# Kernel optimization log

Hardware: AMD Instinct MI355X
Metric: run time of the kernel (lower is better)

Reference implementation:

```python
import jax, jax.numpy as jnp
import numpy as np

N, D_IN, D_OUT, NHEAD = 4096, 512, 128, 4


def setup_inputs() -> dict:
    key = jax.random.key(0)
    k1, k2, k3, k4, k5 = jax.random.split(key, 5)
    adj = jax.random.randint(k1, (N, N), 0, 2).astype(jnp.float32)  # dense binary adjacency
    x = jax.random.normal(k2, (N, D_IN), dtype=jnp.float32)
    W = jax.random.normal(k3, (D_IN, D_OUT), dtype=jnp.float32) * (1.0 / np.sqrt(D_IN))
    attn_l_w = jax.random.normal(k4, (NHEAD, D_OUT), dtype=jnp.float32) * (1.0 / np.sqrt(D_OUT))
    attn_r_w = jax.random.normal(k5, (NHEAD, D_OUT), dtype=jnp.float32) * (1.0 / np.sqrt(D_OUT))
    b = jnp.zeros((D_OUT,), dtype=jnp.float32)
    return {"adj": adj, "x": x, "W": W, "attn_l_w": attn_l_w, "attn_r_w": attn_r_w, "b": b}


def reference(adj, x, W, attn_l_w, attn_r_w, b):
    # h = x @ W : [N, D_OUT]
    h = x @ W
    el = h @ attn_l_w.T  # [N, H]  (nn.Linear(output_dim, nhead, bias=False))
    er = h @ attn_r_w.T  # [N, H]
    # Dense equivalent of nonzero-gather + index_put_ scatter into [N, N, H]:
    # attn[i, j, :] = exp(leaky_relu(el[i] + er[j])) where adj[i, j] != 0, else 0.
    e = el[:, None, :] + er[None, :, :]                      # [N, N, H]
    a = jnp.where(adj[:, :, None] != 0,
                  jnp.exp(jax.nn.leaky_relu(e, negative_slope=0.2)),
                  jnp.zeros((), dtype=e.dtype))              # [N, N, H]
    a = jnp.transpose(a, (0, 2, 1))                          # [N, H, N]
    # F.normalize(p=1, dim=-1): divide by max(L1 row sum, 1e-12); a >= 0 so L1 = sum.
    a = a / jnp.maximum(jnp.sum(a, axis=-1, keepdims=True), 1e-12)
    out = jnp.einsum('nhm,md->nhd', a, h) + b                # [N, H, D_OUT]
    return out.reshape(out.shape[0], -1)                     # flatten heads -> [N, H*D_OUT]
```

## Files before the change

kernel.cpp:

```cpp
#include <hip/hip_runtime.h>

#define NN 4096
#define DIN 512
#define DOUT 128
#define NH 4
#define LOG2E 1.44269504088896340736f

typedef __bf16 bf16x8 __attribute__((ext_vector_type(8)));
typedef float f32x4 __attribute__((ext_vector_type(4)));
typedef float f32x16 __attribute__((ext_vector_type(16)));
typedef unsigned short u16;
typedef unsigned int u32;
typedef u16 u16x8 __attribute__((ext_vector_type(8)));
typedef u16 u16x4 __attribute__((ext_vector_type(4)));

static __device__ __forceinline__ u16 f2bf(float f) {
  __bf16 h = (__bf16)f;
  return __builtin_bit_cast(u16, h);
}

static __device__ __forceinline__ void gl_lds16(const void* g, void* l) {
  __builtin_amdgcn_global_load_lds(
      (const __attribute__((address_space(1))) unsigned int*)g,
      (__attribute__((address_space(3))) unsigned int*)l, 16, 0, 0);
}

__global__ __launch_bounds__(256) void pack_prep(const float* __restrict__ adj,
                                                 u32* __restrict__ adjW,
                                                 const float* __restrict__ W,
                                                 u16* __restrict__ wthi,
                                                 u16* __restrict__ wtlo) {
  const int b = blockIdx.x;
  const int t = threadIdx.x;
  if (b < 2048) {
    const int idx = b * 256 + t;
    const float4* src = (const float4*)(adj + (size_t)idx * 32);
    u32 m = 0;
    #pragma unroll
    for (int c = 0; c < 8; ++c) {
      const float4 v = src[c];
      m |= (v.x != 0.f ? 1u : 0u) << (c * 4);
      m |= (v.y != 0.f ? 2u : 0u) << (c * 4);
      m |= (v.z != 0.f ? 4u : 0u) << (c * 4);
      m |= (v.w != 0.f ? 8u : 0u) << (c * 4);
    }
    adjW[idx] = m;
  } else {
    const int n = b - 2048;
    for (int k = t; k < 512; k += 256) {
      const float w = W[(size_t)k * 128 + n];
      const __bf16 hi = (__bf16)w;
      wthi[(size_t)n * 512 + k] = __builtin_bit_cast(u16, hi);
      wtlo[(size_t)n * 512 + k] = f2bf(w - (float)hi);
    }
  }
}

__global__ __launch_bounds__(512, 1) void hcompute(
    const float* __restrict__ x, const u16* __restrict__ wthi,
    const u16* __restrict__ wtlo, const float* __restrict__ alw,
    const float* __restrict__ arw, u16* __restrict__ hT,
    float* __restrict__ el, float* __restrict__ erT) {
  __shared__ __align__(16) char pool[147456];
  const int t = threadIdx.x;
  const int i0 = blockIdx.x * 16;
  const int lane = t & 63, w = t >> 6;
  const int l15 = lane & 15, lhi = lane >> 4;

  const int xr = t >> 5, xk = (t & 31) * 4;
  const unsigned x_off =
      ((unsigned)(xr * 256 + xk * 2)) ^ ((unsigned)((xr & 7) << 4));

  f32x4 acc = (f32x4){0.f, 0.f, 0.f, 0.f};

  auto stageW = [&](int kc, int buf) {
    #pragma unroll
    for (int q = 0; q < 4; ++q) {
      const int off = q * 8192 + t * 16;
      const int n = off >> 8;
      const int kb = off & 255;
      const int ksrc = (kb ^ ((n & 7) << 4)) >> 1;
      const size_t so = (size_t)n * 512 + kc * 128 + ksrc;
      gl_lds16(wthi + so, pool + 16384 + buf * 32768 + off);
      gl_lds16(wtlo + so, pool + 81920 + buf * 32768 + off);
    }
  };
  auto writeX = [&](const float4& xv, int buf) {
    u16x4 hi, lo;
    const float* xp = (const float*)&xv;
    #pragma unroll
    for (int j = 0; j < 4; ++j) {
      const __bf16 hb = (__bf16)xp[j];
      hi[j] = __builtin_bit_cast(u16, hb);
      lo[j] = f2bf(xp[j] - (float)hb);
    }
    *(u16x4*)(pool + buf * 4096 + x_off) = hi;
    *(u16x4*)(pool + 8192 + buf * 4096 + x_off) = lo;
  };

  stageW(0, 0);
  {
    float4 xv = *(const float4*)(x + (size_t)(i0 + xr) * DIN + xk);
    writeX(xv, 0);
  }
  float4 xnext;
  for (int kc = 0; kc < 4; ++kc) {
    const int cur = kc & 1;
    __syncthreads();
    const bool more = (kc < 3);
    if (more) {
      stageW(kc + 1, cur ^ 1);
      xnext = *(const float4*)(x + (size_t)(i0 + xr) * DIN + (kc + 1) * 128 + xk);
    }
    #pragma unroll
    for (int ks = 0; ks < 4; ++ks) {
      const unsigned kbyte = (unsigned)(ks * 64 + lhi * 16);
      const unsigned xoff =
          (unsigned)(l15 * 256) + (kbyte ^ (unsigned)((l15 & 7) << 4));
      const bf16x8 ah = *(const bf16x8*)(pool + cur * 4096 + xoff);
      const bf16x8 al = *(const bf16x8*)(pool + 8192 + cur * 4096 + xoff);
      const int n = w * 16 + l15;
      const unsigned wb =
          (unsigned)(n * 256) + (kbyte ^ (unsigned)((n & 7) << 4));
      const bf16x8 bh = *(const bf16x8*)(pool + 16384 + cur * 32768 + wb);
      const bf16x8 bl = *(const bf16x8*)(pool + 81920 + cur * 32768 + wb);
      acc = __builtin_amdgcn_mfma_f32_16x16x32_bf16(ah, bh, acc, 0, 0, 0);
      acc = __builtin_amdgcn_mfma_f32_16x16x32_bf16(al, bh, acc, 0, 0, 0);
      acc = __builtin_amdgcn_mfma_f32_16x16x32_bf16(ah, bl, acc, 0, 0, 0);
    }
    if (more) writeX(xnext, cur ^ 1);
  }
  __syncthreads();
  float* h_lds = (float*)(pool + 16384);
  #pragma unroll
  for (int reg = 0; reg < 4; ++reg)
    h_lds[(lhi * 4 + reg) * 132 + w * 16 + l15] = acc[reg];
  __syncthreads();
  {
    const int d = t >> 2, ih0 = (t & 3) * 4;
    u16x4 hv;
    #pragma unroll
    for (int j = 0; j < 4; ++j) hv[j] = f2bf(h_lds[(ih0 + j) * 132 + d]);
    *(u16x4*)(hT + (size_t)d * NN + i0 + ih0) = hv;
  }
  if (t < 128) {
    const int r = t >> 3, hh = (t >> 1) & 3, side = t & 1;
    const float* wrow = (side ? arw : alw) + hh * DOUT;
    float s = 0.f;
    for (int d = 0; d < 128; ++d) s += h_lds[r * 132 + d] * wrow[d];
    s *= LOG2E;
    if (side == 0) el[(size_t)(i0 + r) * NH + hh] = s;
    else erT[(size_t)hh * NN + i0 + r] = s;
  }
}

__global__ __launch_bounds__(512, 1) void gat_main(
    const unsigned char* __restrict__ adjB, const u16* __restrict__ hT,
    const float* __restrict__ el, const float* __restrict__ erT,
    const float* __restrict__ bias, float* __restrict__ outp) {
  __shared__ __align__(16) char B_lds[2][2][16384];
  __shared__ float S_lds[64];
  const int t = threadIdx.x;
  const int i0 = blockIdx.x * 16;
  const int lane = t & 63;
  const int w = t >> 6;
  const int rt = (w >> 2) & 1;
  const int kkg = w & 3;
  const int l31 = lane & 31;
  const int lh = lane >> 5;
  const int il = l31 & 15;
  const int head = rt * 2 + (l31 >> 4);
  const float elv = el[(size_t)(i0 + il) * NH + head];
  if (t < 64) S_lds[t] = 0.f;

  const int bd = t >> 3;
  const int bkb = (t & 7) * 16;
  const u16* hsrc0 = hT + (size_t)bd * NN + (((unsigned)bkb ^ ((bd & 7) << 4)) >> 1);
  const u16* hsrc1 = hsrc0 + (size_t)64 * NN;
  auto stageB = [&](int tile, char* buf) {
    gl_lds16(hsrc0 + tile * 64, buf + t * 16);
    gl_lds16(hsrc1 + tile * 64, buf + 8192 + t * 16);
  };

  const unsigned char* adjp = adjB + (size_t)(i0 + il) * 512 + kkg * 2 + lh;
  const float* erp = erT + (size_t)head * NN + kkg * 16 + lh * 8;
  auto loadInputs = [&](int tile0, float4 (&e0)[2], float4 (&e1)[2], u32 (&ab)[2]) {
    #pragma unroll
    for (int s = 0; s < 2; ++s) {
      e0[s] = *(const float4*)(erp + (tile0 + s) * 64);
      e1[s] = *(const float4*)(erp + (tile0 + s) * 64 + 4);
      ab[s] = adjp[(tile0 + s) * 8];
    }
  };

  f32x16 acc[4];
  #pragma unroll
  for (int ct = 0; ct < 4; ++ct)
    #pragma unroll
    for (int q = 0; q < 16; ++q) acc[ct][q] = 0.f;
  float Sp = 0.f;
  const unsigned kb = (unsigned)(kkg * 32 + lh * 16);

  float4 e0A[2], e1A[2];
  u32 abA[2];
  float4 e0B[2], e1B[2];
  u32 abB[2];
  loadInputs(0, e0A, e1A, abA);
  stageB(0, &B_lds[0][0][0]);
  stageB(1, &B_lds[0][1][0]);

  auto phase = [&](int p, float4 (&ue0)[2], float4 (&ue1)[2], u32 (&uab)[2],
                   float4 (&ne0)[2], float4 (&ne1)[2], u32 (&nab)[2]) {
    const int bp = p & 1;
    __syncthreads();
    if (p < 31) {
      stageB(2 * p + 2, &B_lds[bp ^ 1][0][0]);
      stageB(2 * p + 3, &B_lds[bp ^ 1][1][0]);
      loadInputs(2 * p + 2, ne0, ne1, nab);
    }
    #pragma unroll
    for (int tl = 0; tl < 2; ++tl) {
      float ev[8];
      *(float4*)ev = ue0[tl];
      *(float4*)(ev + 4) = ue1[tl];
      u16x8 pk;
      float s = 0.f;
      #pragma unroll
      for (int q = 0; q < 8; ++q) {
        const float e = elv + ev[q];
        const float lr = fmaxf(e, 0.2f * e);
        const float ex = __builtin_amdgcn_exp2f(lr);
        const int msk = ((int)(uab[tl] << (31 - q))) >> 31;
        const float av =
            __builtin_bit_cast(float, __builtin_bit_cast(int, ex) & msk);
        s += av;
        pk[q] = f2bf(av);
      }
      Sp += s;
      const bf16x8 af = __builtin_bit_cast(bf16x8, pk);
      const char* Bt = &B_lds[bp][tl][0];
      __builtin_amdgcn_s_setprio(1);
      #pragma unroll
      for (int ct = 0; ct < 4; ++ct) {
        const int col = ct * 32 + l31;
        const bf16x8 bfr = *(const bf16x8*)(
            Bt + col * 128 + (kb ^ ((unsigned)(col & 7) << 4)));
        acc[ct] = __builtin_amdgcn_mfma_f32_32x32x16_bf16(af, bfr, acc[ct], 0, 0, 0);
      }
      __builtin_amdgcn_s_setprio(0);
    }
  };

  for (int pp = 0; pp < 16; ++pp) {
    phase(2 * pp, e0A, e1A, abA, e0B, e1B, abB);
    phase(2 * pp + 1, e0B, e1B, abB, e0A, e1A, abA);
  }

  Sp += __shfl_xor(Sp, 32);
  if (lane < 32) atomicAdd(&S_lds[rt * 32 + l31], Sp);

  float* red = (float*)B_lds;
  auto writeAcc = [&](int r) {
    float* dst = red + r * 4096;
    #pragma unroll
    for (int ct = 0; ct < 4; ++ct)
      #pragma unroll
      for (int q4 = 0; q4 < 4; ++q4) {
        f32x4 v;
        #pragma unroll
        for (int j = 0; j < 4; ++j) v[j] = acc[ct][q4 * 4 + j];
        *(f32x4*)(dst + (ct * 4 + q4) * 256 + lane * 4) = v;
      }
  };
  auto addAcc = [&](int r) {
    const float* srcr = red + r * 4096;
    #pragma unroll
    for (int ct = 0; ct < 4; ++ct)
      #pragma unroll
      for (int q4 = 0; q4 < 4; ++q4) {
        const f32x4 v = *(const f32x4*)(srcr + (ct * 4 + q4) * 256 + lane * 4);
        #pragma unroll
        for (int j = 0; j < 4; ++j) acc[ct][q4 * 4 + j] += v[j];
      }
  };
  __syncthreads();
  if (kkg >= 2) writeAcc(rt * 2 + (kkg - 2));
  __syncthreads();
  if (kkg < 2) addAcc(rt * 2 + kkg);
  __syncthreads();
  if (kkg == 1) writeAcc(rt);
  __syncthreads();
  if (kkg == 0) {
    addAcc(rt);
    #pragma unroll
    for (int ct = 0; ct < 4; ++ct) {
      const int col = ct * 32 + l31;
      const float bb = bias[col];
      #pragma unroll
      for (int reg = 0; reg < 16; ++reg) {
        const int crow = (reg & 3) + 8 * (reg >> 2) + 4 * lh;
        const int mrow = rt * 32 + crow;
        const float inv = 1.f / fmaxf(S_lds[mrow], 1e-12f);
        outp[(size_t)(i0 + (mrow & 15)) * (NH * DOUT) + (mrow >> 4) * DOUT + col] =
            acc[ct][reg] * inv + bb;
      }
    }
  }
}

extern "C" void kernel_launch(void* const* d_in, const int* in_sizes, int n_in,
                              void* d_out, int out_size, void* d_ws, size_t ws_size,
                              hipStream_t stream) {
  const float* adj = (const float*)d_in[0];
  const float* x = (const float*)d_in[1];
  const float* W = (const float*)d_in[2];
  const float* alw = (const float*)d_in[3];
  const float* arw = (const float*)d_in[4];
  const float* bias = (const float*)d_in[5];
  float* out = (float*)d_out;
  char* ws = (char*)d_ws;
  u16* hT = (u16*)ws;
  float* el = (float*)(ws + 0x100000);
  float* erT = (float*)(ws + 0x110000);
  unsigned char* adjB = (unsigned char*)(ws + 0x120000);
  u16* wthi = (u16*)(ws + 0x320000);
  u16* wtlo = (u16*)(ws + 0x340000);

  pack_prep<<<2176, 256, 0, stream>>>(adj, (u32*)adjB, W, wthi, wtlo);
  hcompute<<<256, 512, 0, stream>>>(x, wthi, wtlo, alw, arw, hT, el, erT);
  gat_main<<<256, 512, 0, stream>>>(adjB, hT, el, erT, bias, out);
}
```

Before: 172.5 us.

## Factor exp of leaky-relu into products, prepack h fragments, ballot-pack adjacency

The attention weight exp2(leaky(el+er)) is rewritten as max(P_i*Q_j, p_i*q_j), with the exponentials precomputed per node in hcompute. This removes the per-element exp from the main loop. The h matrix is written in MFMA-fragment order so gat_main loads B operands straight from global memory into registers instead of staging through LDS with barriers. Row sums come from an extra MFMA against a ones vector, the adjacency bit-packing uses wave ballots, and launch bounds now allow two blocks per CU. The risks are overflow or precision changes from multiplying exponentials, more global traffic per wave, and higher register pressure.

After: 180.1 us. 4.4% more time.

```diff
diff --git a/kernel.cpp b/kernel.cpp
--- a/kernel.cpp
+++ b/kernel.cpp
@@ -11,6 +11,7 @@
 typedef float f32x16 __attribute__((ext_vector_type(16)));
 typedef unsigned short u16;
 typedef unsigned int u32;
+typedef unsigned long long u64;
 typedef u16 u16x8 __attribute__((ext_vector_type(8)));
 typedef u16 u16x4 __attribute__((ext_vector_type(4)));
 
@@ -26,25 +27,23 @@
 }
 
 __global__ __launch_bounds__(256) void pack_prep(const float* __restrict__ adj,
-                                                 u32* __restrict__ adjW,
+                                                 u64* __restrict__ adjW,
                                                  const float* __restrict__ W,
                                                  u16* __restrict__ wthi,
                                                  u16* __restrict__ wtlo) {
   const int b = blockIdx.x;
   const int t = threadIdx.x;
   if (b < 2048) {
-    const int idx = b * 256 + t;
-    const float4* src = (const float4*)(adj + (size_t)idx * 32);
-    u32 m = 0;
-    #pragma unroll
-    for (int c = 0; c < 8; ++c) {
-      const float4 v = src[c];
-      m |= (v.x != 0.f ? 1u : 0u) << (c * 4);
-      m |= (v.y != 0.f ? 2u : 0u) << (c * 4);
-      m |= (v.z != 0.f ? 4u : 0u) << (c * 4);
-      m |= (v.w != 0.f ? 8u : 0u) << (c * 4);
-    }
-    adjW[idx] = m;
+    const int wv = t >> 6, lane = t & 63;
+    const int gw = b * 4 + wv;
+    const int r = gw >> 1, hf = gw & 1;
+    const float* src = adj + (size_t)r * NN + hf * 2048 + lane;
+    u64* dstw = adjW + (size_t)r * 64 + hf * 32;
+    #pragma unroll 4
+    for (int it = 0; it < 32; ++it) {
+      const u64 m = __ballot(src[it * 64] != 0.f);
+      if (lane == 0) dstw[it] = m;
+    }
   } else {
     const int n = b - 2048;
     for (int k = t; k < 512; k += 256) {
@@ -59,8 +58,9 @@
 __global__ __launch_bounds__(512, 1) void hcompute(
     const float* __restrict__ x, const u16* __restrict__ wthi,
     const u16* __restrict__ wtlo, const float* __restrict__ alw,
-    const float* __restrict__ arw, u16* __restrict__ hT,
-    float* __restrict__ el, float* __restrict__ erT) {
+    const float* __restrict__ arw, u16x8* __restrict__ hTf,
+    float* __restrict__ elP, float* __restrict__ elp,
+    float* __restrict__ erQ, float* __restrict__ erq) {
   __shared__ __align__(16) char pool[147456];
   const int t = threadIdx.x;
   const int i0 = blockIdx.x * 16;
@@ -136,12 +136,18 @@
   for (int reg = 0; reg < 4; ++reg)
     h_lds[(lhi * 4 + reg) * 132 + w * 16 + l15] = acc[reg];
   __syncthreads();
-  {
-    const int d = t >> 2, ih0 = (t & 3) * 4;
-    u16x4 hv;
-    #pragma unroll
-    for (int j = 0; j < 4; ++j) hv[j] = f2bf(h_lds[(ih0 + j) * 132 + d]);
-    *(u16x4*)(hT + (size_t)d * NN + i0 + ih0) = hv;
+  if (t < 256) {
+    const int d = t >> 1, c8 = t & 1;
+    const int j0 = c8 * 8;
+    u16x8 hv;
+    #pragma unroll
+    for (int q = 0; q < 8; ++q) hv[q] = f2bf(h_lds[(j0 + q) * 132 + d]);
+    const int jt = i0 >> 6;
+    const int w8 = ((i0 >> 3) & 7) + c8;
+    const int kt = w8 >> 1, lb = w8 & 1;
+    const int ct = d >> 5;
+    const int l = lb * 32 + (d & 31);
+    hTf[(size_t)((jt * 16 + ct * 4 + kt) * 64 + l)] = hv;
   }
   if (t < 128) {
     const int r = t >> 3, hh = (t >> 1) & 3, side = t & 1;
@@ -149,16 +155,23 @@
     float s = 0.f;
     for (int d = 0; d < 128; ++d) s += h_lds[r * 132 + d] * wrow[d];
     s *= LOG2E;
-    if (side == 0) el[(size_t)(i0 + r) * NH + hh] = s;
-    else erT[(size_t)hh * NN + i0 + r] = s;
-  }
-}
-
-__global__ __launch_bounds__(512, 1) void gat_main(
-    const unsigned char* __restrict__ adjB, const u16* __restrict__ hT,
-    const float* __restrict__ el, const float* __restrict__ erT,
+    const float e1 = exp2f(s), e2 = exp2f(0.2f * s);
+    if (side == 0) {
+      elP[(size_t)(i0 + r) * NH + hh] = e1;
+      elp[(size_t)(i0 + r) * NH + hh] = e2;
+    } else {
+      erQ[(size_t)hh * NN + i0 + r] = e1;
+      erq[(size_t)hh * NN + i0 + r] = e2;
+    }
+  }
+}
+
+__global__ __launch_bounds__(512, 2) void gat_main(
+    const unsigned char* __restrict__ adjB, const u16x8* __restrict__ Bf,
+    const float* __restrict__ elP, const float* __restrict__ elp,
+    const float* __restrict__ erQ, const float* __restrict__ erq,
     const float* __restrict__ bias, float* __restrict__ outp) {
-  __shared__ __align__(16) char B_lds[2][2][16384];
+  __shared__ float red[2][4096];
   __shared__ float S_lds[64];
   const int t = threadIdx.x;
   const int i0 = blockIdx.x * 16;
@@ -170,141 +183,138 @@
   const int lh = lane >> 5;
   const int il = l31 & 15;
   const int head = rt * 2 + (l31 >> 4);
-  const float elv = el[(size_t)(i0 + il) * NH + head];
   if (t < 64) S_lds[t] = 0.f;
-
-  const int bd = t >> 3;
-  const int bkb = (t & 7) * 16;
-  const u16* hsrc0 = hT + (size_t)bd * NN + (((unsigned)bkb ^ ((bd & 7) << 4)) >> 1);
-  const u16* hsrc1 = hsrc0 + (size_t)64 * NN;
-  auto stageB = [&](int tile, char* buf) {
-    gl_lds16(hsrc0 + tile * 64, buf + t * 16);
-    gl_lds16(hsrc1 + tile * 64, buf + 8192 + t * 16);
-  };
-
+  __syncthreads();
+  const float Pv = elP[(size_t)(i0 + il) * NH + head];
+  const float pv = elp[(size_t)(i0 + il) * NH + head];
   const unsigned char* adjp = adjB + (size_t)(i0 + il) * 512 + kkg * 2 + lh;
-  const float* erp = erT + (size_t)head * NN + kkg * 16 + lh * 8;
-  auto loadInputs = [&](int tile0, float4 (&e0)[2], float4 (&e1)[2], u32 (&ab)[2]) {
-    #pragma unroll
-    for (int s = 0; s < 2; ++s) {
-      e0[s] = *(const float4*)(erp + (tile0 + s) * 64);
-      e1[s] = *(const float4*)(erp + (tile0 + s) * 64 + 4);
-      ab[s] = adjp[(tile0 + s) * 8];
-    }
-  };
-
-  f32x16 acc[4];
+  const float* Qp = erQ + (size_t)head * NN + kkg * 16 + lh * 8;
+  const float* qp = erq + (size_t)head * NN + kkg * 16 + lh * 8;
+  const int fbase = kkg * 64 + lane;
+
+  f32x16 acc0, acc1, acc2, acc3, accS;
   #pragma unroll
-  for (int ct = 0; ct < 4; ++ct)
-    #pragma unroll
-    for (int q = 0; q < 16; ++q) acc[ct][q] = 0.f;
-  float Sp = 0.f;
-  const unsigned kb = (unsigned)(kkg * 32 + lh * 16);
-
-  float4 e0A[2], e1A[2];
-  u32 abA[2];
-  float4 e0B[2], e1B[2];
-  u32 abB[2];
-  loadInputs(0, e0A, e1A, abA);
-  stageB(0, &B_lds[0][0][0]);
-  stageB(1, &B_lds[0][1][0]);
-
-  auto phase = [&](int p, float4 (&ue0)[2], float4 (&ue1)[2], u32 (&uab)[2],
-                   float4 (&ne0)[2], float4 (&ne1)[2], u32 (&nab)[2]) {
-    const int bp = p & 1;
-    __syncthreads();
-    if (p < 31) {
-      stageB(2 * p + 2, &B_lds[bp ^ 1][0][0]);
-      stageB(2 * p + 3, &B_lds[bp ^ 1][1][0]);
-      loadInputs(2 * p + 2, ne0, ne1, nab);
-    }
-    #pragma unroll
-    for (int tl = 0; tl < 2; ++tl) {
-      float ev[8];
-      *(float4*)ev = ue0[tl];
-      *(float4*)(ev + 4) = ue1[tl];
-      u16x8 pk;
-      float s = 0.f;
-      #pragma unroll
-      for (int q = 0; q < 8; ++q) {
-        const float e = elv + ev[q];
-        const float lr = fmaxf(e, 0.2f * e);
-        const float ex = __builtin_amdgcn_exp2f(lr);
-        const int msk = ((int)(uab[tl] << (31 - q))) >> 31;
-        const float av =
-            __builtin_bit_cast(float, __builtin_bit_cast(int, ex) & msk);
-        s += av;
-        pk[q] = f2bf(av);
-      }
-      Sp += s;
-      const bf16x8 af = __builtin_bit_cast(bf16x8, pk);
-      const char* Bt = &B_lds[bp][tl][0];
-      __builtin_amdgcn_s_setprio(1);
-      #pragma unroll
-      for (int ct = 0; ct < 4; ++ct) {
-        const int col = ct * 32 + l31;
-        const bf16x8 bfr = *(const bf16x8*)(
-            Bt + col * 128 + (kb ^ ((unsigned)(col & 7) << 4)));
-        acc[ct] = __builtin_amdgcn_mfma_f32_32x32x16_bf16(af, bfr, acc[ct], 0, 0, 0);
-      }
-      __builtin_amdgcn_s_setprio(0);
-    }
-  };
-
-  for (int pp = 0; pp < 16; ++pp) {
-    phase(2 * pp, e0A, e1A, abA, e0B, e1B, abB);
-    phase(2 * pp + 1, e0B, e1B, abB, e0A, e1A, abA);
-  }
-
-  Sp += __shfl_xor(Sp, 32);
-  if (lane < 32) atomicAdd(&S_lds[rt * 32 + l31], Sp);
-
-  float* red = (float*)B_lds;
-  auto writeAcc = [&](int r) {
-    float* dst = red + r * 4096;
-    #pragma unroll
-    for (int ct = 0; ct < 4; ++ct)
-      #pragma unroll
-      for (int q4 = 0; q4 < 4; ++q4) {
-        f32x4 v;
-        #pragma unroll
-        for (int j = 0; j < 4; ++j) v[j] = acc[ct][q4 * 4 + j];
-        *(f32x4*)(dst + (ct * 4 + q4) * 256 + lane * 4) = v;
-      }
-  };
-  auto addAcc = [&](int r) {
-    const float* srcr = red + r * 4096;
-    #pragma unroll
-    for (int ct = 0; ct < 4; ++ct)
-      #pragma unroll
-      for (int q4 = 0; q4 < 4; ++q4) {
-        const f32x4 v = *(const f32x4*)(srcr + (ct * 4 + q4) * 256 + lane * 4);
-        #pragma unroll
-        for (int j = 0; j < 4; ++j) acc[ct][q4 * 4 + j] += v[j];
-      }
-  };
-  __syncthreads();
-  if (kkg >= 2) writeAcc(rt * 2 + (kkg - 2));
-  __syncthreads();
-  if (kkg < 2) addAcc(rt * 2 + kkg);
-  __syncthreads();
-  if (kkg == 1) writeAcc(rt);
-  __syncthreads();
+  for (int q = 0; q < 16; ++q) {
+    acc0[q] = 0.f; acc1[q] = 0.f; acc2[q] = 0.f; acc3[q] = 0.f; accS[q] = 0.f;
+  }
+  u16x8 onesu;
+  #pragma unroll
+  for (int q = 0; q < 8; ++q) onesu[q] = 0x3F80;
+  const bf16x8 onesf = __builtin_bit_cast(bf16x8, onesu);
+
+  auto loadP = [&](int jt, float4& Q0, float4& Q1, float4& q0, float4& q1,
+                   u32& ab, u16x8& b0, u16x8& b1, u16x8& b2, u16x8& b3) {
+    const float* Qj = Qp + jt * 64;
+    const float* qj = qp + jt * 64;
+    Q0 = *(const float4*)Qj;
+    Q1 = *(const float4*)(Qj + 4);
+    q0 = *(const float4*)qj;
+    q1 = *(const float4*)(qj + 4);
+    ab = adjp[jt * 8];
+    const u16x8* fb = Bf + jt * 1024 + fbase;
+    b0 = fb[0];
+    b1 = fb[256];
+    b2 = fb[512];
+    b3 = fb[768];
+  };
+  auto computeP = [&](const float4& Q0, const float4& Q1, const float4& q0,
+                      const float4& q1, u32 ab, const u16x8& b0,
+                      const u16x8& b1, const u16x8& b2, const u16x8& b3) {
+    float Qv[8], qv[8];
+    *(float4*)Qv = Q0;
+    *(float4*)(Qv + 4) = Q1;
+    *(float4*)qv = q0;
+    *(float4*)(qv + 4) = q1;
+    u16x8 pk;
+    #pragma unroll
+    for (int q = 0; q < 8; ++q) {
+      const float v = fmaxf(Pv * Qv[q], pv * qv[q]);
+      const int msk = ((int)(ab << (31 - q))) >> 31;
+      pk[q] = f2bf(__builtin_bit_cast(float, __builtin_bit_cast(int, v) & msk));
+    }
+    const bf16x8 af = __builtin_bit_cast(bf16x8, pk);
+    __builtin_amdgcn_s_setprio(1);
+    accS = __builtin_amdgcn_mfma_f32_32x32x16_bf16(af, onesf, accS, 0, 0, 0);
+    acc0 = __builtin_amdgcn_mfma_f32_32x32x16_bf16(
+        af, __builtin_bit_cast(bf16x8, b0), acc0, 0, 0, 0);
+    acc1 = __builtin_amdgcn_mfma_f32_32x32x16_bf16(
+        af, __builtin_bit_cast(bf16x8, b1), acc1, 0, 0, 0);
+    acc2 = __builtin_amdgcn_mfma_f32_32x32x16_bf16(
+        af, __builtin_bit_cast(bf16x8, b2), acc2, 0, 0, 0);
+    acc3 = __builtin_amdgcn_mfma_f32_32x32x16_bf16(
+        af, __builtin_bit_cast(bf16x8, b3), acc3, 0, 0, 0);
+    __builtin_amdgcn_s_setprio(0);
+  };
+
+  float4 Q0A, Q1A, q0A, q1A, Q0B, Q1B, q0B, q1B;
+  u32 abA, abB;
+  u16x8 b0A, b1A, b2A, b3A, b0B, b1B, b2B, b3B;
+  loadP(0, Q0A, Q1A, q0A, q1A, abA, b0A, b1A, b2A, b3A);
+  for (int pp = 0; pp < 32; ++pp) {
+    loadP(2 * pp + 1, Q0B, Q1B, q0B, q1B, abB, b0B, b1B, b2B, b3B);
+    computeP(Q0A, Q1A, q0A, q1A, abA, b0A, b1A, b2A, b3A);
+    if (pp < 31)
+      loadP(2 * pp + 2, Q0A, Q1A, q0A, q1A, abA, b0A, b1A, b2A, b3A);
+    computeP(Q0B, Q1B, q0B, q1B, abB, b0B, b1B, b2B, b3B);
+  }
+
+  if (l31 == 0) {
+    #pragma unroll
+    for (int reg = 0; reg < 16; ++reg) {
+      const int crow = (reg & 3) + 8 * (reg >> 2) + 4 * lh;
+      atomicAdd(&S_lds[rt * 32 + crow], accS[reg]);
+    }
+  }
+  auto wr1 = [&](f32x16& a, int ct) {
+    float* dst = red[rt] + ct * 1024 + lane * 4;
+    #pragma unroll
+    for (int q4 = 0; q4 < 4; ++q4)
+      *(f32x4*)(dst + q4 * 256) =
+          (f32x4){a[q4 * 4], a[q4 * 4 + 1], a[q4 * 4 + 2], a[q4 * 4 + 3]};
+  };
+  auto ad1 = [&](f32x16& a, int ct) {
+    const float* s = red[rt] + ct * 1024 + lane * 4;
+    #pragma unroll
+    for (int q4 = 0; q4 < 4; ++q4) {
+      const f32x4 v = *(const f32x4*)(s + q4 * 256);
+      a[q4 * 4] += v[0];
+      a[q4 * 4 + 1] += v[1];
+      a[q4 * 4 + 2] += v[2];
+      a[q4 * 4 + 3] += v[3];
+    }
+  };
+  auto writeAcc = [&]() { wr1(acc0, 0); wr1(acc1, 1); wr1(acc2, 2); wr1(acc3, 3); };
+  auto addAcc = [&]() { ad1(acc0, 0); ad1(acc1, 1); ad1(acc2, 2); ad1(acc3, 3); };
+
+  __syncthreads();
+  if (kkg == 1) writeAcc();
+  __syncthreads();
+  if (kkg == 0) addAcc();
+  __syncthreads();
+  if (kkg == 3) writeAcc();
+  __syncthreads();
+  if (kkg == 2) addAcc();
+  __syncthreads();
+  if (kkg == 2) writeAcc();
+  __syncthreads();
+  auto st1 = [&](f32x16& a, int ct) {
+    const int col = ct * 32 + l31;
+    const float bb = bias[col];
+    #pragma unroll
+    for (int reg = 0; reg < 16; ++reg) {
+      const int crow = (reg & 3) + 8 * (reg >> 2) + 4 * lh;
+      const int mrow = rt * 32 + crow;
+      const float inv = 1.f / fmaxf(S_lds[mrow], 1e-12f);
+      outp[(size_t)(i0 + (mrow & 15)) * (NH * DOUT) + (mrow >> 4) * DOUT + col] =
+          a[reg] * inv + bb;
+    }
+  };
   if (kkg == 0) {
-    addAcc(rt);
-    #pragma unroll
-    for (int ct = 0; ct < 4; ++ct) {
-      const int col = ct * 32 + l31;
-      const float bb = bias[col];
-      #pragma unroll
-      for (int reg = 0; reg < 16; ++reg) {
-        const int crow = (reg & 3) + 8 * (reg >> 2) + 4 * lh;
-        const int mrow = rt * 32 + crow;
-        const float inv = 1.f / fmaxf(S_lds[mrow], 1e-12f);
-        outp[(size_t)(i0 + (mrow & 15)) * (NH * DOUT) + (mrow >> 4) * DOUT + col] =
-            acc[ct][reg] * inv + bb;
-      }
-    }
+    addAcc();
+    st1(acc0, 0);
+    st1(acc1, 1);
+    st1(acc2, 2);
+    st1(acc3, 3);
   }
 }
 
@@ -319,14 +329,17 @@
   const float* bias = (const float*)d_in[5];
   float* out = (float*)d_out;
   char* ws = (char*)d_ws;
-  u16* hT = (u16*)ws;
-  float* el = (float*)(ws + 0x100000);
-  float* erT = (float*)(ws + 0x110000);
-  unsigned char* adjB = (unsigned char*)(ws + 0x120000);
-  u16* wthi = (u16*)(ws + 0x320000);
-  u16* wtlo = (u16*)(ws + 0x340000);
-
-  pack_prep<<<2176, 256, 0, stream>>>(adj, (u32*)adjB, W, wthi, wtlo);
-  hcompute<<<256, 512, 0, stream>>>(x, wthi, wtlo, alw, arw, hT, el, erT);
-  gat_main<<<256, 512, 0, stream>>>(adjB, hT, el, erT, bias, out);
-}
+  u16x8* hTf = (u16x8*)ws;
+  float* elP = (float*)(ws + 0x100000);
+  float* elp = (float*)(ws + 0x110000);
+  float* erQ = (float*)(ws + 0x120000);
+  float* erq = (float*)(ws + 0x130000);
+  unsigned char* adjB = (unsigned char*)(ws + 0x140000);
+  u16* wthi = (u16*)(ws + 0x340000);
+  u16* wtlo = (u16*)(ws + 0x360000);
+
+  pack_prep<<<2176, 256, 0, stream>>>(adj, (u64*)adjB, W, wthi, wtlo);
+  hcompute<<<256, 512, 0, stream>>>(x, wthi, wtlo, alw, arw, hTf, elP, elp, erQ, erq);
+  gat_main<<<256, 512, 0, stream>>>(adjB, (const u16x8*)hTf, elP, elp, erQ, erq,
+                                    bias, out);
+}
```
